# Kernel optimization log

Hardware: AMD Instinct MI355X
Metric: run time of the kernel (lower is better)

The kernel has to match this reference:

```python
import jax, jax.numpy as jnp
import numpy as np

TEMPERATURE = 0.5
EPS = 1e-20


def setup_inputs() -> dict:
    key = jax.random.key(0)
    ks = jax.random.split(key, 7)
    N, T, S = 16, 64, 1024
    SRC, TGT, D = 512, 512, 64
    return {
        "input": jax.random.normal(ks[0], (N, T, TGT), jnp.float32),
        "memory_bank": jax.random.normal(ks[1], (N, S, SRC), jnp.float32),
        "W_q": jax.random.normal(ks[2], (TGT, D), jnp.float32) / np.sqrt(TGT),
        "W_ctx": jax.random.normal(ks[3], (SRC, D), jnp.float32) / np.sqrt(SRC),
        "v": jax.random.normal(ks[4], (D,), jnp.float32) / np.sqrt(D),
        "W_out": jax.random.normal(ks[5], (SRC + TGT, TGT), jnp.float32) / np.sqrt(SRC + TGT),
        "b_out": jax.random.normal(ks[6], (TGT,), jnp.float32) * 0.01,
    }


def reference(input, memory_bank, W_q, W_ctx, v, W_out, b_out):
    # MLP attention score: v^T tanh(W_q q + W_ctx h)
    wq = jnp.einsum("ntd,de->nte", input, W_q)            # [N,T,D]
    uh = jnp.einsum("nsd,de->nse", memory_bank, W_ctx)    # [N,S,D]
    wquh = jnp.tanh(wq[:, :, None, :] + uh[:, None, :, :])  # [N,T,S,D]
    scores = jnp.einsum("ntsd,d->nts", wquh, v)           # [N,T,S]

    log_alpha = jax.nn.log_softmax(scores, axis=-1)
    alpha = jnp.exp(log_alpha)                            # c_align_vectors

    # deterministic context + output
    context_c = jnp.einsum("nts,nsd->ntd", alpha, memory_bank)
    h_c = jnp.tanh(jnp.concatenate([input, context_c], axis=-1) @ W_out + b_out)

    # gumbel-softmax sample (K = n_samples = 1, forced by view_as in original)
    u = jax.random.uniform(jax.random.key(42), log_alpha.shape, jnp.float32)
    g = -jnp.log(-jnp.log(u + EPS) + EPS)                 # gumbel noise
    y_align = jax.nn.softmax((log_alpha + g) / TEMPERATURE, axis=-1)  # [N,T,S]

    context_y = jnp.einsum("nts,nsd->ntd", y_align, memory_bank)
    h_y = jnp.tanh(jnp.concatenate([input, context_y], axis=-1) @ W_out + b_out)

    return jnp.stack([h_c, h_y], axis=0)  # [2,N,T,tgt_dim]
```

## Files before the change

kernel.cpp:

```cpp
#include <hip/hip_runtime.h>
#include <hip/hip_bf16.h>
#include <stdint.h>

#define DEV __device__ __forceinline__

typedef __attribute__((ext_vector_type(8))) short short8;
typedef __attribute__((ext_vector_type(4))) float f32x4;

#define TWO_LOG2E 2.8853900817779268f

DEV unsigned short f2bf(float f) {
  uint32_t u = __float_as_uint(f);
  u += 0x7FFFu + ((u >> 16) & 1u);
  return (unsigned short)(u >> 16);
}

DEV uint2 pk4(float4 f) {
  union { __hip_bfloat162 h; unsigned u; } a, b;
  a.h = __float22bfloat162_rn(make_float2(f.x, f.y));
  b.h = __float22bfloat162_rn(make_float2(f.z, f.w));
  return make_uint2(a.u, b.u);
}

DEV short8 mk8(uint2 lo, uint2 hi) {
  union { short8 s; uint4 u; } t;
  t.u = make_uint4(lo.x, lo.y, hi.x, hi.y);
  return t.s;
}

DEV uint32_t rotl32(uint32_t x, int r) { return (x << r) | (x >> (32 - r)); }

DEV void threefry_0_42(uint32_t x0, uint32_t x1, uint32_t& o0, uint32_t& o1) {
  const uint32_t ks0 = 0u, ks1 = 42u, ks2 = 0x1BD11BDAu ^ 42u;
  x0 += ks0; x1 += ks1;
#define TFR(r) { x0 += x1; x1 = rotl32(x1, (r)); x1 ^= x0; }
  TFR(13) TFR(15) TFR(26) TFR(6)  x0 += ks1; x1 += ks2 + 1u;
  TFR(17) TFR(29) TFR(16) TFR(24) x0 += ks2; x1 += ks0 + 2u;
  TFR(13) TFR(15) TFR(26) TFR(6)  x0 += ks0; x1 += ks1 + 3u;
  TFR(17) TFR(29) TFR(16) TFR(24) x0 += ks1; x1 += ks2 + 4u;
  TFR(13) TFR(15) TFR(26) TFR(6)  x0 += ks2; x1 += ks0 + 5u;
#undef TFR
  o0 = x0; o1 = x1;
}

DEV float wredmax(float v) {
#pragma unroll
  for (int off = 32; off > 0; off >>= 1) v = fmaxf(v, __shfl_xor(v, off));
  return v;
}
DEV float wredsum(float v) {
#pragma unroll
  for (int off = 32; off > 0; off >>= 1) v += __shfl_xor(v, off);
  return v;
}

DEV void ph_transpose(int b, int tid, char* smem,
                      const float* Wctx, const float* Wq, const float* Wout,
                      unsigned short* WctxT, unsigned short* WqT, unsigned short* WoutT) {
  float (*tile)[65] = (float(*)[65])smem;
  const float* src; unsigned short* dst; int R, C, br, bc;
  if (b < 8)       { src = Wctx; dst = WctxT; R = 512;  C = 64;  br = b * 64;       bc = 0; }
  else if (b < 16) { src = Wq;   dst = WqT;   R = 512;  C = 64;  br = (b - 8) * 64; bc = 0; }
  else { int i = b - 16; src = Wout; dst = WoutT; R = 1024; C = 512; br = (i & 15) * 64; bc = (i >> 4) * 64; }
  const int lr = tid >> 4, lc4 = (tid & 15) * 4;
#pragma unroll
  for (int i = 0; i < 4; ++i) {
    float4 vv = *(const float4*)(src + (long)(br + lr + i * 16) * C + bc + lc4);
    tile[lr + i * 16][lc4 + 0] = vv.x;
    tile[lr + i * 16][lc4 + 1] = vv.y;
    tile[lr + i * 16][lc4 + 2] = vv.z;
    tile[lr + i * 16][lc4 + 3] = vv.w;
  }
  __syncthreads();
#pragma unroll
  for (int i = 0; i < 4; ++i) {
    int crow = lr + i * 16;
    ushort4 o;
    o.x = f2bf(tile[lc4 + 0][crow]);
    o.y = f2bf(tile[lc4 + 1][crow]);
    o.z = f2bf(tile[lc4 + 2][crow]);
    o.w = f2bf(tile[lc4 + 3][crow]);
    *(ushort4*)(dst + (long)(bc + crow) * R + br + lc4) = o;
  }
}

DEV void ph_mbtile(int i, int tid, char* smem, const float* mb, unsigned short* mbT) {
  float (*tile)[65] = (float(*)[65])smem;
  const int n = i >> 7, rem = i & 127;
  const int sr0 = (rem >> 3) * 64;
  const int c0 = (rem & 7) * 64;
  const int lr = tid >> 4, lc4 = (tid & 15) * 4;
#pragma unroll
  for (int k = 0; k < 4; ++k) {
    float4 vv = *(const float4*)(mb + ((long)n * 1024 + sr0 + lr + k * 16) * 512 + c0 + lc4);
    tile[lr + k * 16][lc4 + 0] = vv.x;
    tile[lr + k * 16][lc4 + 1] = vv.y;
    tile[lr + k * 16][lc4 + 2] = vv.z;
    tile[lr + k * 16][lc4 + 3] = vv.w;
  }
  __syncthreads();
#pragma unroll
  for (int k = 0; k < 4; ++k) {
    int crow = lr + k * 16;
    ushort4 o;
    o.x = f2bf(tile[lc4 + 0][crow]);
    o.y = f2bf(tile[lc4 + 1][crow]);
    o.z = f2bf(tile[lc4 + 2][crow]);
    o.w = f2bf(tile[lc4 + 3][crow]);
    *(ushort4*)(mbT + (long)n * 524288 + (long)(c0 + crow) * 1024 + sr0 + lc4) = o;
  }
}

DEV void ph_uhwq(int t, int tid, char* smem,
                 const float* mb, const float* input,
                 const unsigned short* WctxT, const unsigned short* WqT,
                 float* uhT, float* wqo) {
  unsigned short (*As)[32] = (unsigned short(*)[32])smem;
  unsigned short (*Bs)[32] = (unsigned short(*)[32])(smem + 4096);
  const float* A; const unsigned short* BT; int mbase;
  if (t < 256) { A = mb;    BT = WctxT; mbase = t * 64; }
  else         { A = input; BT = WqT;   mbase = (t - 256) * 64; }
  const int srow = tid >> 2, kc = tid & 3;
  const int scol = ((kc ^ (srow & 3)) * 8);
  const int wave = tid >> 6, lane = tid & 63;
  const int wm = (wave >> 1) * 32, wn = (wave & 1) * 32;
  const int q = lane >> 4, r = lane & 15;
  const int c0 = ((q ^ (r & 3)) * 8);
  const float* ap = A + (long)(mbase + srow) * 512 + kc * 8;
  const unsigned short* bp = BT + (long)srow * 512 + kc * 8;
  f32x4 acc[2][2];
#pragma unroll
  for (int i = 0; i < 2; ++i)
#pragma unroll
    for (int j = 0; j < 2; ++j) acc[i][j] = (f32x4){0.f, 0.f, 0.f, 0.f};
  float4 fa0 = *(const float4*)(ap);
  float4 fa1 = *(const float4*)(ap + 4);
  uint4 fb = *(const uint4*)(bp);
  for (int k0 = 0; k0 < 512; k0 += 32) {
    uint2 p0 = pk4(fa0), p1 = pk4(fa1);
    *(uint4*)&As[srow][scol] = make_uint4(p0.x, p0.y, p1.x, p1.y);
    *(uint4*)&Bs[srow][scol] = fb;
    __syncthreads();
    if (k0 + 32 < 512) {
      fa0 = *(const float4*)(ap + k0 + 32);
      fa1 = *(const float4*)(ap + k0 + 36);
      fb = *(const uint4*)(bp + k0 + 32);
    }
    short8 a0 = *(const short8*)&As[wm + r][c0];
    short8 a1 = *(const short8*)&As[wm + 16 + r][c0];
    short8 b0 = *(const short8*)&Bs[wn + r][c0];
    short8 b1 = *(const short8*)&Bs[wn + 16 + r][c0];
    acc[0][0] = __builtin_amdgcn_mfma_f32_16x16x32_bf16(a0, b0, acc[0][0], 0, 0, 0);
    acc[0][1] = __builtin_amdgcn_mfma_f32_16x16x32_bf16(a0, b1, acc[0][1], 0, 0, 0);
    acc[1][0] = __builtin_amdgcn_mfma_f32_16x16x32_bf16(a1, b0, acc[1][0], 0, 0, 0);
    acc[1][1] = __builtin_amdgcn_mfma_f32_16x16x32_bf16(a1, b1, acc[1][1], 0, 0, 0);
    __syncthreads();
  }
#pragma unroll
  for (int i2 = 0; i2 < 2; ++i2)
#pragma unroll
    for (int j2 = 0; j2 < 2; ++j2) {
      int gcol = wn + j2 * 16 + r;
      int m = mbase + wm + i2 * 16 + q * 4;
      if (t < 256) {
        int n = m >> 10, s0 = m & 1023;
        float4 o;
        o.x = acc[i2][j2][0] * TWO_LOG2E;
        o.y = acc[i2][j2][1] * TWO_LOG2E;
        o.z = acc[i2][j2][2] * TWO_LOG2E;
        o.w = acc[i2][j2][3] * TWO_LOG2E;
        *(float4*)(uhT + (long)n * 65536 + (long)gcol * 1024 + s0) = o;
      } else {
#pragma unroll
        for (int reg = 0; reg < 4; ++reg)
          wqo[(long)(m + reg) * 64 + gcol] = acc[i2][j2][reg] * TWO_LOG2E;
      }
    }
}

DEV void ph_pre(int tt, int tid, char* smem,
                const float* input, const unsigned short* WoutT,
                const float* bout, float* P) {
  unsigned short (*As)[32] = (unsigned short(*)[32])smem;
  unsigned short (*Bs)[32] = (unsigned short(*)[32])(smem + 4096);
  const int mbase = (tt >> 4) * 64, nbase = (tt & 15) * 32;
  const int srow = tid >> 2, kc = tid & 3;
  const int scol = ((kc ^ (srow & 3)) * 8);
  const int wave = tid >> 6, lane = tid & 63;
  const int wm = (wave >> 1) * 32, wn = (wave & 1) * 16;
  const int q = lane >> 4, r = lane & 15;
  const int c0 = ((q ^ (r & 3)) * 8);
  const float* ap = input + (long)(mbase + srow) * 512 + kc * 8;
  const int brow = (tid & 127) >> 2;
  const unsigned short* bp = WoutT + (long)(nbase + brow) * 1024 + kc * 8;
  f32x4 acc[2];
  acc[0] = (f32x4){0.f, 0.f, 0.f, 0.f};
  acc[1] = (f32x4){0.f, 0.f, 0.f, 0.f};
  float4 fa0 = *(const float4*)(ap);
  float4 fa1 = *(const float4*)(ap + 4);
  uint4 fb;
  if (tid < 128) fb = *(const uint4*)(bp);
  for (int k0 = 0; k0 < 512; k0 += 32) {
    uint2 p0 = pk4(fa0), p1 = pk4(fa1);
    *(uint4*)&As[srow][scol] = make_uint4(p0.x, p0.y, p1.x, p1.y);
    if (tid < 128) *(uint4*)&Bs[brow][(kc ^ (brow & 3)) * 8] = fb;
    __syncthreads();
    int kn = k0 + 32;
    if (kn < 512) {
      fa0 = *(const float4*)(ap + kn);
      fa1 = *(const float4*)(ap + kn + 4);
      if (tid < 128) fb = *(const uint4*)(bp + kn);
    }
    short8 a0 = *(const short8*)&As[wm + r][c0];
    short8 a1 = *(const short8*)&As[wm + 16 + r][c0];
    short8 b0 = *(const short8*)&Bs[wn + r][c0];
    acc[0] = __builtin_amdgcn_mfma_f32_16x16x32_bf16(a0, b0, acc[0], 0, 0, 0);
    acc[1] = __builtin_amdgcn_mfma_f32_16x16x32_bf16(a1, b0, acc[1], 0, 0, 0);
    __syncthreads();
  }
#pragma unroll
  for (int i2 = 0; i2 < 2; ++i2) {
    int gcol = nbase + wn + r;
    float bb = bout[gcol];
#pragma unroll
    for (int reg = 0; reg < 4; ++reg) {
      int grow = mbase + wm + i2 * 16 + q * 4 + reg;
      P[(long)grow * 512 + gcol] = acc[i2][reg] + bb;
    }
  }
}

DEV void softmax_gumbel_write(float* lsc, int nt, int tid, float* red,
                              unsigned short* alpha_bf, unsigned short* yal_bf) {
  const int wv = tid >> 6, ln = tid & 63;
  float m = fmaxf(fmaxf(lsc[0], lsc[1]), fmaxf(lsc[2], lsc[3]));
  m = wredmax(m);
  if (ln == 0) red[wv] = m;
  __syncthreads();
  m = fmaxf(fmaxf(red[0], red[1]), fmaxf(red[2], red[3]));
  __syncthreads();
  float ss = 0.f;
#pragma unroll
  for (int i = 0; i < 4; ++i) ss += __expf(lsc[i] - m);
  ss = wredsum(ss);
  if (ln == 0) red[wv] = ss;
  __syncthreads();
  ss = red[0] + red[1] + red[2] + red[3];
  const float logl = __logf(ss);
  __syncthreads();

  const uint32_t jbase = (uint32_t)nt * 1024u + (uint32_t)tid * 4u;
  float ys[4];
  float4 av;
#pragma unroll
  for (int i = 0; i < 4; ++i) {
    float la = lsc[i] - m - logl;
    ((float*)&av)[i] = __expf(la);
    uint32_t o0, o1;
    threefry_0_42(0u, jbase + i, o0, o1);
    uint32_t bits = o0 ^ o1;
    float u = __uint_as_float((bits >> 9) | 0x3f800000u) - 1.0f;
    float g = -__logf(-__logf(u + 1e-20f) + 1e-20f);
    ys[i] = (la + g) * 2.0f;
  }
  {
    uint2 pa = pk4(av);
    *(uint2*)(alpha_bf + (long)nt * 1024 + tid * 4) = pa;
  }
  float m2 = fmaxf(fmaxf(ys[0], ys[1]), fmaxf(ys[2], ys[3]));
  m2 = wredmax(m2);
  if (ln == 0) red[wv] = m2;
  __syncthreads();
  m2 = fmaxf(fmaxf(red[0], red[1]), fmaxf(red[2], red[3]));
  __syncthreads();
  float s2 = 0.f;
  float4 ye;
#pragma unroll
  for (int i = 0; i < 4; ++i) { ((float*)&ye)[i] = __expf(ys[i] - m2); s2 += ((float*)&ye)[i]; }
  s2 = wredsum(s2);
  if (ln == 0) red[wv] = s2;
  __syncthreads();
  s2 = red[0] + red[1] + red[2] + red[3];
  const float rinv = __fdividef(1.f, s2);
  ye.x *= rinv; ye.y *= rinv; ye.z *= rinv; ye.w *= rinv;
  {
    uint2 py = pk4(ye);
    *(uint2*)(yal_bf + (long)nt * 1024 + tid * 4) = py;
  }
  __syncthreads();
}

DEV void ph_scores_pair(int nt0, int tid, char* smem,
                        const float* uhT, const float* wqo, const float* vvec,
                        unsigned short* alpha_bf, unsigned short* yal_bf) {
  float* wvs0 = (float*)smem;
  float* wvs1 = wvs0 + 64;
  float* vvs  = wvs1 + 64;
  float* red  = vvs + 64;
  const int nt1 = nt0 + 512;
  const int n0 = nt0 >> 6, n1 = nt1 >> 6;
  if (tid < 64) {
    wvs0[tid] = wqo[nt0 * 64 + tid];
    wvs1[tid] = wqo[nt1 * 64 + tid];
    vvs[tid]  = vvec[tid];
  }
  __syncthreads();
  float sumv = 0.f;
#pragma unroll
  for (int d = 0; d < 64; d += 4) {
    float4 vv = *(const float4*)&vvs[d];
    sumv += vv.x + vv.y + vv.z + vv.w;
  }
  const float* un0 = uhT + (long)n0 * 65536 + tid * 4;
  const float* un1 = uhT + (long)n1 * 65536 + tid * 4;
  float4 r0 = make_float4(0.f, 0.f, 0.f, 0.f);
  float4 r1 = make_float4(0.f, 0.f, 0.f, 0.f);
  for (int db = 0; db < 64; db += 4) {
    float4 ua[4], ub[4];
#pragma unroll
    for (int j = 0; j < 4; ++j) {
      ua[j] = *(const float4*)(un0 + (long)(db + j) * 1024);
      ub[j] = *(const float4*)(un1 + (long)(db + j) * 1024);
    }
#pragma unroll
    for (int j = 0; j < 4; ++j) {
      float w0 = wvs0[db + j], w1 = wvs1[db + j], vvj = vvs[db + j];
      r0.x = fmaf(vvj, __builtin_amdgcn_rcpf(1.f + __builtin_amdgcn_exp2f(ua[j].x + w0)), r0.x);
      r0.y = fmaf(vvj, __builtin_amdgcn_rcpf(1.f + __builtin_amdgcn_exp2f(ua[j].y + w0)), r0.y);
      r0.z = fmaf(vvj, __builtin_amdgcn_rcpf(1.f + __builtin_amdgcn_exp2f(ua[j].z + w0)), r0.z);
      r0.w = fmaf(vvj, __builtin_amdgcn_rcpf(1.f + __builtin_amdgcn_exp2f(ua[j].w + w0)), r0.w);
      r1.x = fmaf(vvj, __builtin_amdgcn_rcpf(1.f + __builtin_amdgcn_exp2f(ub[j].x + w1)), r1.x);
      r1.y = fmaf(vvj, __builtin_amdgcn_rcpf(1.f + __builtin_amdgcn_exp2f(ub[j].y + w1)), r1.y);
      r1.z = fmaf(vvj, __builtin_amdgcn_rcpf(1.f + __builtin_amdgcn_exp2f(ub[j].z + w1)), r1.z);
      r1.w = fmaf(vvj, __builtin_amdgcn_rcpf(1.f + __builtin_amdgcn_exp2f(ub[j].w + w1)), r1.w);
    }
  }
  float lsc0[4], lsc1[4];
  lsc0[0] = fmaf(-2.f, r0.x, sumv); lsc0[1] = fmaf(-2.f, r0.y, sumv);
  lsc0[2] = fmaf(-2.f, r0.z, sumv); lsc0[3] = fmaf(-2.f, r0.w, sumv);
  lsc1[0] = fmaf(-2.f, r1.x, sumv); lsc1[1] = fmaf(-2.f, r1.y, sumv);
  lsc1[2] = fmaf(-2.f, r1.z, sumv); lsc1[3] = fmaf(-2.f, r1.w, sumv);
  softmax_gumbel_write(lsc0, nt0, tid, red, alpha_bf, yal_bf);
  softmax_gumbel_write(lsc1, nt1, tid, red, alpha_bf, yal_bf);
}

DEV void ph_ctx_fast(int n, int dbase, int vt, int tid, char* smem,
                     const unsigned short* alpha_bf, const unsigned short* yal_bf,
                     const unsigned short* mbT, unsigned short* ctxb) {
  unsigned short (*As)[32] = (unsigned short(*)[32])smem;
  const int srow = tid >> 2, kc = tid & 3;
  const int scol = ((kc ^ (srow & 3)) * 8);
  const int wave = tid >> 6, lane = tid & 63;
  const int wm = (wave >> 1) * 32, wn = (wave & 1) * 16;
  const int q = lane >> 4, r = lane & 15;
  const int c0 = ((q ^ (r & 3)) * 8);
  const unsigned short* Ab = (vt ? yal_bf : alpha_bf) + (long)n * 65536 + (long)srow * 1024 + kc * 8;
  const unsigned short* Bb = mbT + (long)n * 524288 + (long)(dbase + wn + r) * 1024 + q * 8;
  f32x4 acc[2];
  acc[0] = (f32x4){0.f, 0.f, 0.f, 0.f};
  acc[1] = (f32x4){0.f, 0.f, 0.f, 0.f};
  uint4 fa  = *(const uint4*)(Ab);
  uint4 fb0 = *(const uint4*)(Bb);
  uint4 fb1 = *(const uint4*)(Bb + 32);
  for (int k0 = 0; k0 < 1024; k0 += 32) {
    *(uint4*)&As[srow][scol] = fa;
    __syncthreads();
    union { uint4 u; short8 s; } bu; bu.u = fb0;
    if (k0 + 32 < 1024) fa = *(const uint4*)(Ab + k0 + 32);
    fb0 = fb1;
    if (k0 + 64 < 1024) fb1 = *(const uint4*)(Bb + k0 + 64);
    short8 a0 = *(const short8*)&As[wm + r][c0];
    short8 a1 = *(const short8*)&As[wm + 16 + r][c0];
    acc[0] = __builtin_amdgcn_mfma_f32_16x16x32_bf16(a0, bu.s, acc[0], 0, 0, 0);
    acc[1] = __builtin_amdgcn_mfma_f32_16x16x32_bf16(a1, bu.s, acc[1], 0, 0, 0);
    __syncthreads();
  }
#pragma unroll
  for (int i2 = 0; i2 < 2; ++i2) {
    int gcol = dbase + wn + r;
#pragma unroll
    for (int reg = 0; reg < 4; ++reg) {
      long grow = (long)vt * 1024 + n * 64 + wm + i2 * 16 + q * 4 + reg;
      ctxb[grow * 512 + gcol] = f2bf(acc[i2][reg]);
    }
  }
}

DEV void ph_ctx_legacy(int n, int dbase, int vt, int tid, char* smem,
                       const unsigned short* alpha_bf, const unsigned short* yal_bf,
                       const float* mb, unsigned short* ctxb) {
  unsigned short (*As)[32] = (unsigned short(*)[32])smem;
  const int srow = tid >> 2, kc = tid & 3;
  const int scol = ((kc ^ (srow & 3)) * 8);
  const int wave = tid >> 6, lane = tid & 63;
  const int wm = (wave >> 1) * 32, wn = (wave & 1) * 16;
  const int q = lane >> 4, r = lane & 15;
  const int c0 = ((q ^ (r & 3)) * 8);
  const unsigned short* Ab = (vt ? yal_bf : alpha_bf) + (long)n * 65536 + (long)srow * 1024 + kc * 8;
  const float* bcol = mb + (long)n * 524288 + dbase + wn + r;
  f32x4 acc[2];
  acc[0] = (f32x4){0.f, 0.f, 0.f, 0.f};
  acc[1] = (f32x4){0.f, 0.f, 0.f, 0.f};
  uint4 fa = *(const uint4*)(Ab);
  float bv[8];
#pragma unroll
  for (int j = 0; j < 8; ++j) bv[j] = bcol[(long)(q * 8 + j) * 512];
  for (int k0 = 0; k0 < 1024; k0 += 32) {
    *(uint4*)&As[srow][scol] = fa;
    __syncthreads();
    float4 blo = make_float4(bv[0], bv[1], bv[2], bv[3]);
    float4 bhi = make_float4(bv[4], bv[5], bv[6], bv[7]);
    short8 b0 = mk8(pk4(blo), pk4(bhi));
    if (k0 + 32 < 1024) {
      fa = *(const uint4*)(Ab + k0 + 32);
#pragma unroll
      for (int j = 0; j < 8; ++j) bv[j] = bcol[(long)(k0 + 32 + q * 8 + j) * 512];
    }
    short8 a0 = *(const short8*)&As[wm + r][c0];
    short8 a1 = *(const short8*)&As[wm + 16 + r][c0];
    acc[0] = __builtin_amdgcn_mfma_f32_16x16x32_bf16(a0, b0, acc[0], 0, 0, 0);
    acc[1] = __builtin_amdgcn_mfma_f32_16x16x32_bf16(a1, b0, acc[1], 0, 0, 0);
    __syncthreads();
  }
#pragma unroll
  for (int i2 = 0; i2 < 2; ++i2) {
    int gcol = dbase + wn + r;
#pragma unroll
    for (int reg = 0; reg < 4; ++reg) {
      long grow = (long)vt * 1024 + n * 64 + wm + i2 * 16 + q * 4 + reg;
      ctxb[grow * 512 + gcol] = f2bf(acc[i2][reg]);
    }
  }
}

DEV void ph_out(int mbase, int nbase, int tid, char* smem,
                const unsigned short* ctxb, const unsigned short* WoutT,
                const float* P, float* out) {
  unsigned short (*As)[32] = (unsigned short(*)[32])smem;
  unsigned short (*Bs)[32] = (unsigned short(*)[32])(smem + 4096);
  const int srow = tid >> 2, kc = tid & 3;
  const int scol = ((kc ^ (srow & 3)) * 8);
  const int wave = tid >> 6, lane = tid & 63;
  const int wm = (wave >> 1) * 32, wn = (wave & 1) * 16;
  const int q = lane >> 4, r = lane & 15;
  const int c0 = ((q ^ (r & 3)) * 8);
  const unsigned short* ap = ctxb + (long)(mbase + srow) * 512 + kc * 8;
  const int brow = (tid & 127) >> 2;
  const unsigned short* bp = WoutT + (long)(nbase + brow) * 1024 + 512 + kc * 8;
  f32x4 acc[2];
#pragma unroll
  for (int i2 = 0; i2 < 2; ++i2) {
    int pcol = nbase + wn + r;
#pragma unroll
    for (int reg = 0; reg < 4; ++reg) {
      int prow = (mbase + wm + i2 * 16 + q * 4 + reg) & 1023;
      acc[i2][reg] = P[(long)prow * 512 + pcol];
    }
  }
  uint4 fa = *(const uint4*)(ap);
  uint4 fb;
  if (tid < 128) fb = *(const uint4*)(bp);
  for (int k0 = 0; k0 < 512; k0 += 32) {
    *(uint4*)&As[srow][scol] = fa;
    if (tid < 128) *(uint4*)&Bs[brow][(kc ^ (brow & 3)) * 8] = fb;
    __syncthreads();
    int kn = k0 + 32;
    if (kn < 512) {
      fa = *(const uint4*)(ap + kn);
      if (tid < 128) fb = *(const uint4*)(bp + kn);
    }
    short8 a0 = *(const short8*)&As[wm + r][c0];
    short8 a1 = *(const short8*)&As[wm + 16 + r][c0];
    short8 b0 = *(const short8*)&Bs[wn + r][c0];
    acc[0] = __builtin_amdgcn_mfma_f32_16x16x32_bf16(a0, b0, acc[0], 0, 0, 0);
    acc[1] = __builtin_amdgcn_mfma_f32_16x16x32_bf16(a1, b0, acc[1], 0, 0, 0);
    __syncthreads();
  }
#pragma unroll
  for (int i2 = 0; i2 < 2; ++i2) {
    int gcol = nbase + wn + r;
#pragma unroll
    for (int reg = 0; reg < 4; ++reg) {
      int grow = mbase + wm + i2 * 16 + q * 4 + reg;
      float z = acc[i2][reg];
      float rc = __builtin_amdgcn_rcpf(1.f + __builtin_amdgcn_exp2f(z * TWO_LOG2E));
      out[(long)grow * 512 + gcol] = fmaf(-2.f, rc, 1.f);
    }
  }
}

__global__ __launch_bounds__(256) void k_prep(const float* __restrict__ Wctx,
                                              const float* __restrict__ Wq,
                                              const float* __restrict__ Wout,
                                              const float* __restrict__ mb,
                                              unsigned short* __restrict__ WctxT,
                                              unsigned short* __restrict__ WqT,
                                              unsigned short* __restrict__ WoutT,
                                              unsigned short* __restrict__ mbT) {
  __shared__ __align__(16) char smem[16640];
  const int b = blockIdx.x;
  if (b < 144) ph_transpose(b, threadIdx.x, smem, Wctx, Wq, Wout, WctxT, WqT, WoutT);
  else         ph_mbtile(b - 144, threadIdx.x, smem, mb, mbT);
}

__global__ __launch_bounds__(256) void k_uhwq_pre(const float* __restrict__ mb,
                                                  const float* __restrict__ input,
                                                  const unsigned short* __restrict__ WctxT,
                                                  const unsigned short* __restrict__ WqT,
                                                  const unsigned short* __restrict__ WoutT,
                                                  const float* __restrict__ bout,
                                                  float* __restrict__ uhT,
                                                  float* __restrict__ wqo,
                                                  float* __restrict__ P) {
  __shared__ __align__(16) char smem[8192];
  const int b = blockIdx.x;
  if (b < 272) ph_uhwq(b, threadIdx.x, smem, mb, input, WctxT, WqT, uhT, wqo);
  else         ph_pre(b - 272, threadIdx.x, smem, input, WoutT, bout, P);
}

__global__ __launch_bounds__(256) void k_scores(const float* __restrict__ uhT,
                                                const float* __restrict__ wqo,
                                                const float* __restrict__ vvec,
                                                unsigned short* __restrict__ alpha_bf,
                                                unsigned short* __restrict__ yal_bf) {
  __shared__ __align__(16) char smem[1024];
  ph_scores_pair(blockIdx.x, threadIdx.x, smem, uhT, wqo, vvec, alpha_bf, yal_bf);
}

__global__ __launch_bounds__(256) void k_ctx_fast(const unsigned short* __restrict__ alpha_bf,
                                                  const unsigned short* __restrict__ yal_bf,
                                                  const unsigned short* __restrict__ mbT,
                                                  unsigned short* __restrict__ ctxb) {
  __shared__ __align__(16) char smem[4096];
  const int x = blockIdx.x;
  ph_ctx_fast(x & 15, ((x >> 4) & 15) * 32, x >> 8, threadIdx.x, smem, alpha_bf, yal_bf, mbT, ctxb);
}

__global__ __launch_bounds__(256) void k_ctx_legacy(const unsigned short* __restrict__ alpha_bf,
                                                    const unsigned short* __restrict__ yal_bf,
                                                    const float* __restrict__ mb,
                                                    unsigned short* __restrict__ ctxb) {
  __shared__ __align__(16) char smem[4096];
  const int x = blockIdx.x;
  ph_ctx_legacy(x & 15, ((x >> 4) & 15) * 32, x >> 8, threadIdx.x, smem, alpha_bf, yal_bf, mb, ctxb);
}

__global__ __launch_bounds__(256) void k_out(const unsigned short* __restrict__ ctxb,
                                             const unsigned short* __restrict__ WoutT,
                                             const float* __restrict__ P,
                                             float* __restrict__ out) {
  __shared__ __align__(16) char smem[8192];
  ph_out((blockIdx.x >> 4) * 64, (blockIdx.x & 15) * 32, threadIdx.x, smem, ctxb, WoutT, P, out);
}

extern "C" void kernel_launch(void* const* d_in, const int* in_sizes, int n_in,
                              void* d_out, int out_size, void* d_ws, size_t ws_size,
                              hipStream_t stream) {
  const float* input = (const float*)d_in[0];
  const float* mb    = (const float*)d_in[1];
  const float* W_q   = (const float*)d_in[2];
  const float* W_ctx = (const float*)d_in[3];
  const float* v     = (const float*)d_in[4];
  const float* W_out = (const float*)d_in[5];
  const float* b_out = (const float*)d_in[6];
  float* out = (float*)d_out;
  float* ws = (float*)d_ws;

  float* uhT = ws;
  float* wqo = ws + 1048576;
  unsigned short* alpha_bf = (unsigned short*)(ws + 1114112);
  unsigned short* yal_bf   = (unsigned short*)(ws + 1638400);
  unsigned short* WctxT = (unsigned short*)(ws + 2162688);
  unsigned short* WqT   = (unsigned short*)(ws + 2179072);
  unsigned short* WoutT = (unsigned short*)(ws + 2195456);
  unsigned short* ctxb  = (unsigned short*)(ws + 2457600);
  float* P = ws + 2981888;
  unsigned short* mbT = (unsigned short*)(ws + 3506176);

  const bool big = ws_size >= (size_t)7700480 * 4;

  k_prep<<<big ? 2192 : 144, 256, 0, stream>>>(W_ctx, W_q, W_out, mb, WctxT, WqT, WoutT, mbT);
  k_uhwq_pre<<<528, 256, 0, stream>>>(mb, input, WctxT, WqT, WoutT, b_out, uhT, wqo, P);
  k_scores<<<512, 256, 0, stream>>>(uhT, wqo, v, alpha_bf, yal_bf);
  if (big) k_ctx_fast<<<512, 256, 0, stream>>>(alpha_bf, yal_bf, mbT, ctxb);
  else     k_ctx_legacy<<<512, 256, 0, stream>>>(alpha_bf, yal_bf, mb, ctxb);
  k_out<<<512, 256, 0, stream>>>(ctxb, WoutT, P, out);
}
```

Baseline: 147.6 us.

## Pre-convert inputs to bf16 and stage GEMM tiles via async global-to-LDS double buffering

```diff
diff --git a/kernel.cpp b/kernel.cpp
--- a/kernel.cpp
+++ b/kernel.cpp
@@ -8,6 +8,7 @@
 typedef __attribute__((ext_vector_type(4))) float f32x4;
 
 #define TWO_LOG2E 2.8853900817779268f
+#define MFMA16(a, b, c) __builtin_amdgcn_mfma_f32_16x16x32_bf16((a), (b), (c), 0, 0, 0)
 
 DEV unsigned short f2bf(float f) {
   uint32_t u = __float_as_uint(f);
@@ -20,12 +21,6 @@
   a.h = __float22bfloat162_rn(make_float2(f.x, f.y));
   b.h = __float22bfloat162_rn(make_float2(f.z, f.w));
   return make_uint2(a.u, b.u);
-}
-
-DEV short8 mk8(uint2 lo, uint2 hi) {
-  union { short8 s; uint4 u; } t;
-  t.u = make_uint4(lo.x, lo.y, hi.x, hi.y);
-  return t.s;
 }
 
 DEV uint32_t rotl32(uint32_t x, int r) { return (x << r) | (x >> (32 - r)); }
@@ -54,6 +49,34 @@
   return v;
 }
 
+DEV void gld16(const unsigned short* g, unsigned short* l) {
+  __builtin_amdgcn_global_load_lds(
+      (__attribute__((address_space(1))) void*)g,
+      (__attribute__((address_space(3))) void*)l, 16, 0, 0);
+}
+
+DEV void stage64(const unsigned short* src, long lda, int k0,
+                 unsigned short* buf, int tid) {
+  const int srow = tid >> 2;
+  const int sc = (((tid & 3) ^ (srow & 3)) * 8);
+  const int wave = tid >> 6;
+  const unsigned short* g = src + (long)srow * lda + k0 + sc;
+  gld16(g,      buf + wave * 512);
+  gld16(g + 32, buf + 2048 + wave * 512);
+}
+
+DEV void stage32(const unsigned short* src, long lda, int k0,
+                 unsigned short* buf, int tid) {
+  const int wave = tid >> 6, lane = tid & 63;
+  const int h = wave >> 1;
+  const int row = ((wave & 1) << 4) + (lane >> 2);
+  const int sc = (((lane & 3) ^ (row & 3)) * 8);
+  gld16(src + (long)row * lda + k0 + h * 32 + sc,
+        buf + h * 1024 + (wave & 1) * 512);
+}
+
+#define RD8(buf, row, col) (*(const short8*)&(buf)[(row) * 32 + (col)])
+
 DEV void ph_transpose(int b, int tid, char* smem,
                       const float* Wctx, const float* Wq, const float* Wout,
                       unsigned short* WctxT, unsigned short* WqT, unsigned short* WoutT) {
@@ -84,7 +107,8 @@
   }
 }
 
-DEV void ph_mbtile(int i, int tid, char* smem, const float* mb, unsigned short* mbT) {
+DEV void ph_mbtile(int i, int tid, char* smem, const float* mb,
+                   unsigned short* mbT, unsigned short* mb_bf) {
   float (*tile)[65] = (float(*)[65])smem;
   const int n = i >> 7, rem = i & 127;
   const int sr0 = (rem >> 3) * 64;
@@ -92,11 +116,15 @@
   const int lr = tid >> 4, lc4 = (tid & 15) * 4;
 #pragma unroll
   for (int k = 0; k < 4; ++k) {
-    float4 vv = *(const float4*)(mb + ((long)n * 1024 + sr0 + lr + k * 16) * 512 + c0 + lc4);
+    const long srow = (long)n * 1024 + sr0 + lr + k * 16;
+    float4 vv = *(const float4*)(mb + srow * 512 + c0 + lc4);
     tile[lr + k * 16][lc4 + 0] = vv.x;
     tile[lr + k * 16][lc4 + 1] = vv.y;
     tile[lr + k * 16][lc4 + 2] = vv.z;
     tile[lr + k * 16][lc4 + 3] = vv.w;
+    ushort4 o;
+    o.x = f2bf(vv.x); o.y = f2bf(vv.y); o.z = f2bf(vv.z); o.w = f2bf(vv.w);
+    *(ushort4*)(mb_bf + srow * 512 + c0 + lc4) = o;
   }
   __syncthreads();
 #pragma unroll
@@ -111,121 +139,142 @@
   }
 }
 
-DEV void ph_uhwq(int t, int tid, char* smem,
-                 const float* mb, const float* input,
-                 const unsigned short* WctxT, const unsigned short* WqT,
-                 float* uhT, float* wqo) {
-  unsigned short (*As)[32] = (unsigned short(*)[32])smem;
-  unsigned short (*Bs)[32] = (unsigned short(*)[32])(smem + 4096);
-  const float* A; const unsigned short* BT; int mbase;
-  if (t < 256) { A = mb;    BT = WctxT; mbase = t * 64; }
-  else         { A = input; BT = WqT;   mbase = (t - 256) * 64; }
-  const int srow = tid >> 2, kc = tid & 3;
-  const int scol = ((kc ^ (srow & 3)) * 8);
+DEV void ph_inpconv(int i, int tid, const float* input, unsigned short* input_bf) {
+  const long base = (long)i * 8192 + (long)tid * 32;
+#pragma unroll
+  for (int j = 0; j < 32; j += 4) {
+    float4 vv = *(const float4*)(input + base + j);
+    uint2 p = pk4(vv);
+    *(uint2*)(input_bf + base + j) = p;
+  }
+}
+
+__global__ __launch_bounds__(256) void k_prep(const float* __restrict__ Wctx,
+                                              const float* __restrict__ Wq,
+                                              const float* __restrict__ Wout,
+                                              const float* __restrict__ mb,
+                                              const float* __restrict__ input,
+                                              unsigned short* __restrict__ WctxT,
+                                              unsigned short* __restrict__ WqT,
+                                              unsigned short* __restrict__ WoutT,
+                                              unsigned short* __restrict__ mbT,
+                                              unsigned short* __restrict__ mb_bf,
+                                              unsigned short* __restrict__ input_bf) {
+  __shared__ __align__(16) char smem[16640];
+  const int b = blockIdx.x;
+  if (b < 144)       ph_transpose(b, threadIdx.x, smem, Wctx, Wq, Wout, WctxT, WqT, WoutT);
+  else if (b < 2192) ph_mbtile(b - 144, threadIdx.x, smem, mb, mbT, mb_bf);
+  else               ph_inpconv(b - 2192, threadIdx.x, input, input_bf);
+}
+
+__global__ __launch_bounds__(256) void k_gemms(const unsigned short* __restrict__ mb_bf,
+                                               const unsigned short* __restrict__ input_bf,
+                                               const unsigned short* __restrict__ WctxT,
+                                               const unsigned short* __restrict__ WqT,
+                                               const unsigned short* __restrict__ WoutT,
+                                               const float* __restrict__ bout,
+                                               float* __restrict__ uhT,
+                                               float* __restrict__ wqo,
+                                               float* __restrict__ P) {
+  __shared__ __align__(16) unsigned short Ab[8192];
+  __shared__ __align__(16) unsigned short Bb[8192];
+  const int tid = threadIdx.x;
+  const int t = blockIdx.x;
   const int wave = tid >> 6, lane = tid & 63;
-  const int wm = (wave >> 1) * 32, wn = (wave & 1) * 32;
   const int q = lane >> 4, r = lane & 15;
   const int c0 = ((q ^ (r & 3)) * 8);
-  const float* ap = A + (long)(mbase + srow) * 512 + kc * 8;
-  const unsigned short* bp = BT + (long)srow * 512 + kc * 8;
-  f32x4 acc[2][2];
-#pragma unroll
-  for (int i = 0; i < 2; ++i)
-#pragma unroll
-    for (int j = 0; j < 2; ++j) acc[i][j] = (f32x4){0.f, 0.f, 0.f, 0.f};
-  float4 fa0 = *(const float4*)(ap);
-  float4 fa1 = *(const float4*)(ap + 4);
-  uint4 fb = *(const uint4*)(bp);
-  for (int k0 = 0; k0 < 512; k0 += 32) {
-    uint2 p0 = pk4(fa0), p1 = pk4(fa1);
-    *(uint4*)&As[srow][scol] = make_uint4(p0.x, p0.y, p1.x, p1.y);
-    *(uint4*)&Bs[srow][scol] = fb;
-    __syncthreads();
-    if (k0 + 32 < 512) {
-      fa0 = *(const float4*)(ap + k0 + 32);
-      fa1 = *(const float4*)(ap + k0 + 36);
-      fb = *(const uint4*)(bp + k0 + 32);
-    }
-    short8 a0 = *(const short8*)&As[wm + r][c0];
-    short8 a1 = *(const short8*)&As[wm + 16 + r][c0];
-    short8 b0 = *(const short8*)&Bs[wn + r][c0];
-    short8 b1 = *(const short8*)&Bs[wn + 16 + r][c0];
-    acc[0][0] = __builtin_amdgcn_mfma_f32_16x16x32_bf16(a0, b0, acc[0][0], 0, 0, 0);
-    acc[0][1] = __builtin_amdgcn_mfma_f32_16x16x32_bf16(a0, b1, acc[0][1], 0, 0, 0);
-    acc[1][0] = __builtin_amdgcn_mfma_f32_16x16x32_bf16(a1, b0, acc[1][0], 0, 0, 0);
-    acc[1][1] = __builtin_amdgcn_mfma_f32_16x16x32_bf16(a1, b1, acc[1][1], 0, 0, 0);
-    __syncthreads();
-  }
-#pragma unroll
-  for (int i2 = 0; i2 < 2; ++i2)
-#pragma unroll
-    for (int j2 = 0; j2 < 2; ++j2) {
-      int gcol = wn + j2 * 16 + r;
-      int m = mbase + wm + i2 * 16 + q * 4;
-      if (t < 256) {
-        int n = m >> 10, s0 = m & 1023;
-        float4 o;
-        o.x = acc[i2][j2][0] * TWO_LOG2E;
-        o.y = acc[i2][j2][1] * TWO_LOG2E;
-        o.z = acc[i2][j2][2] * TWO_LOG2E;
-        o.w = acc[i2][j2][3] * TWO_LOG2E;
-        *(float4*)(uhT + (long)n * 65536 + (long)gcol * 1024 + s0) = o;
-      } else {
-#pragma unroll
-        for (int reg = 0; reg < 4; ++reg)
-          wqo[(long)(m + reg) * 64 + gcol] = acc[i2][j2][reg] * TWO_LOG2E;
+
+  if (t < 272) {
+    const unsigned short* Asrc; const unsigned short* Bsrc; int mbase;
+    if (t < 256) { Asrc = mb_bf + (long)t * 32768;          Bsrc = WctxT; mbase = t * 64; }
+    else         { Asrc = input_bf + (long)(t - 256) * 32768; Bsrc = WqT; mbase = (t - 256) * 64; }
+    const int wm = (wave >> 1) * 32, wn = (wave & 1) * 32;
+    f32x4 acc[2][2];
+#pragma unroll
+    for (int i = 0; i < 2; ++i)
+#pragma unroll
+      for (int j = 0; j < 2; ++j) acc[i][j] = (f32x4){0.f, 0.f, 0.f, 0.f};
+    stage64(Asrc, 512, 0, Ab, tid);
+    stage64(Bsrc, 512, 0, Bb, tid);
+    for (int c = 0; c < 8; ++c) {
+      const int db = (c & 1) * 4096;
+      __syncthreads();
+      if (c < 7) {
+        stage64(Asrc, 512, (c + 1) * 64, Ab + (db ^ 4096), tid);
+        stage64(Bsrc, 512, (c + 1) * 64, Bb + (db ^ 4096), tid);
       }
-    }
-}
-
-DEV void ph_pre(int tt, int tid, char* smem,
-                const float* input, const unsigned short* WoutT,
-                const float* bout, float* P) {
-  unsigned short (*As)[32] = (unsigned short(*)[32])smem;
-  unsigned short (*Bs)[32] = (unsigned short(*)[32])(smem + 4096);
-  const int mbase = (tt >> 4) * 64, nbase = (tt & 15) * 32;
-  const int srow = tid >> 2, kc = tid & 3;
-  const int scol = ((kc ^ (srow & 3)) * 8);
-  const int wave = tid >> 6, lane = tid & 63;
-  const int wm = (wave >> 1) * 32, wn = (wave & 1) * 16;
-  const int q = lane >> 4, r = lane & 15;
-  const int c0 = ((q ^ (r & 3)) * 8);
-  const float* ap = input + (long)(mbase + srow) * 512 + kc * 8;
-  const int brow = (tid & 127) >> 2;
-  const unsigned short* bp = WoutT + (long)(nbase + brow) * 1024 + kc * 8;
-  f32x4 acc[2];
-  acc[0] = (f32x4){0.f, 0.f, 0.f, 0.f};
-  acc[1] = (f32x4){0.f, 0.f, 0.f, 0.f};
-  float4 fa0 = *(const float4*)(ap);
-  float4 fa1 = *(const float4*)(ap + 4);
-  uint4 fb;
-  if (tid < 128) fb = *(const uint4*)(bp);
-  for (int k0 = 0; k0 < 512; k0 += 32) {
-    uint2 p0 = pk4(fa0), p1 = pk4(fa1);
-    *(uint4*)&As[srow][scol] = make_uint4(p0.x, p0.y, p1.x, p1.y);
-    if (tid < 128) *(uint4*)&Bs[brow][(kc ^ (brow & 3)) * 8] = fb;
-    __syncthreads();
-    int kn = k0 + 32;
-    if (kn < 512) {
-      fa0 = *(const float4*)(ap + kn);
-      fa1 = *(const float4*)(ap + kn + 4);
-      if (tid < 128) fb = *(const uint4*)(bp + kn);
-    }
-    short8 a0 = *(const short8*)&As[wm + r][c0];
-    short8 a1 = *(const short8*)&As[wm + 16 + r][c0];
-    short8 b0 = *(const short8*)&Bs[wn + r][c0];
-    acc[0] = __builtin_amdgcn_mfma_f32_16x16x32_bf16(a0, b0, acc[0], 0, 0, 0);
-    acc[1] = __builtin_amdgcn_mfma_f32_16x16x32_bf16(a1, b0, acc[1], 0, 0, 0);
-    __syncthreads();
-  }
-#pragma unroll
-  for (int i2 = 0; i2 < 2; ++i2) {
-    int gcol = nbase + wn + r;
-    float bb = bout[gcol];
-#pragma unroll
-    for (int reg = 0; reg < 4; ++reg) {
-      int grow = mbase + wm + i2 * 16 + q * 4 + reg;
-      P[(long)grow * 512 + gcol] = acc[i2][reg] + bb;
+#pragma unroll
+      for (int h = 0; h < 2; ++h) {
+        const unsigned short* A = Ab + db + h * 2048;
+        const unsigned short* B = Bb + db + h * 2048;
+        short8 a0 = RD8(A, wm + r, c0);
+        short8 a1 = RD8(A, wm + 16 + r, c0);
+        short8 b0 = RD8(B, wn + r, c0);
+        short8 b1 = RD8(B, wn + 16 + r, c0);
+        acc[0][0] = MFMA16(a0, b0, acc[0][0]);
+        acc[0][1] = MFMA16(a0, b1, acc[0][1]);
+        acc[1][0] = MFMA16(a1, b0, acc[1][0]);
+        acc[1][1] = MFMA16(a1, b1, acc[1][1]);
+      }
+    }
+#pragma unroll
+    for (int i2 = 0; i2 < 2; ++i2)
+#pragma unroll
+      for (int j2 = 0; j2 < 2; ++j2) {
+        int gcol = wn + j2 * 16 + r;
+        int m = mbase + wm + i2 * 16 + q * 4;
+        if (t < 256) {
+          int n = m >> 10, s0 = m & 1023;
+          float4 o;
+          o.x = acc[i2][j2][0] * TWO_LOG2E;
+          o.y = acc[i2][j2][1] * TWO_LOG2E;
+          o.z = acc[i2][j2][2] * TWO_LOG2E;
+          o.w = acc[i2][j2][3] * TWO_LOG2E;
+          *(float4*)(uhT + (long)n * 65536 + (long)gcol * 1024 + s0) = o;
+        } else {
+#pragma unroll
+          for (int reg = 0; reg < 4; ++reg)
+            wqo[(long)(m + reg) * 64 + gcol] = acc[i2][j2][reg] * TWO_LOG2E;
+        }
+      }
+  } else {
+    const int tt = t - 272;
+    const int mbase = (tt >> 4) * 64, nbase = (tt & 15) * 32;
+    const int wm = (wave >> 1) * 32, wn = (wave & 1) * 16;
+    const unsigned short* Asrc = input_bf + (long)mbase * 512;
+    const unsigned short* Bsrc = WoutT + (long)nbase * 1024;
+    f32x4 acc[2];
+    acc[0] = (f32x4){0.f, 0.f, 0.f, 0.f};
+    acc[1] = (f32x4){0.f, 0.f, 0.f, 0.f};
+    stage64(Asrc, 512, 0, Ab, tid);
+    stage32(Bsrc, 1024, 0, Bb, tid);
+    for (int c = 0; c < 8; ++c) {
+      const int dbA = (c & 1) * 4096, dbB = (c & 1) * 2048;
+      __syncthreads();
+      if (c < 7) {
+        stage64(Asrc, 512, (c + 1) * 64, Ab + (dbA ^ 4096), tid);
+        stage32(Bsrc, 1024, (c + 1) * 64, Bb + (dbB ^ 2048), tid);
+      }
+#pragma unroll
+      for (int h = 0; h < 2; ++h) {
+        const unsigned short* A = Ab + dbA + h * 2048;
+        const unsigned short* B = Bb + dbB + h * 1024;
+        short8 a0 = RD8(A, wm + r, c0);
+        short8 a1 = RD8(A, wm + 16 + r, c0);
+        short8 b0 = RD8(B, wn + r, c0);
+        acc[0] = MFMA16(a0, b0, acc[0]);
+        acc[1] = MFMA16(a1, b0, acc[1]);
+      }
+    }
+#pragma unroll
+    for (int i2 = 0; i2 < 2; ++i2) {
+      int gcol = nbase + wn + r;
+      float bb = bout[gcol];
+#pragma unroll
+      for (int reg = 0; reg < 4; ++reg) {
+        int grow = mbase + wm + i2 * 16 + q * 4 + reg;
+        P[(long)grow * 512 + gcol] = acc[i2][reg] + bb;
+      }
     }
   }
 }
@@ -290,13 +339,19 @@
   __syncthreads();
 }
 
-DEV void ph_scores_pair(int nt0, int tid, char* smem,
-                        const float* uhT, const float* wqo, const float* vvec,
-                        unsigned short* alpha_bf, unsigned short* yal_bf) {
-  float* wvs0 = (float*)smem;
-  float* wvs1 = wvs0 + 64;
-  float* vvs  = wvs1 + 64;
-  float* red  = vvs + 64;
+__global__ __launch_bounds__(256) void k_scores(const float* __restrict__ uhT,
+                                                const float* __restrict__ wqo,
+                                                const float* __restrict__ vvec,
+                                                unsigned short* __restrict__ alpha_bf,
+                                                unsigned short* __restrict__ yal_bf) {
+  __shared__ __align__(16) float smf[196];
+  float* wvs0 = smf;
+  float* wvs1 = smf + 64;
+  float* vvs  = smf + 128;
+  float* red  = smf + 192;
+  const int tid = threadIdx.x;
+  const int bid = blockIdx.x;
+  const int nt0 = ((bid & 7) << 6) | (bid >> 3);
   const int nt1 = nt0 + 512;
   const int n0 = nt0 >> 6, n1 = nt1 >> 6;
   if (tid < 64) {
@@ -344,36 +399,44 @@
   softmax_gumbel_write(lsc1, nt1, tid, red, alpha_bf, yal_bf);
 }
 
-DEV void ph_ctx_fast(int n, int dbase, int vt, int tid, char* smem,
-                     const unsigned short* alpha_bf, const unsigned short* yal_bf,
-                     const unsigned short* mbT, unsigned short* ctxb) {
-  unsigned short (*As)[32] = (unsigned short(*)[32])smem;
-  const int srow = tid >> 2, kc = tid & 3;
-  const int scol = ((kc ^ (srow & 3)) * 8);
+__global__ __launch_bounds__(256) void k_ctx(const unsigned short* __restrict__ alpha_bf,
+                                             const unsigned short* __restrict__ yal_bf,
+                                             const unsigned short* __restrict__ mbT,
+                                             unsigned short* __restrict__ ctxb) {
+  __shared__ __align__(16) unsigned short Ab[8192];
+  const int tid = threadIdx.x;
+  const int x = blockIdx.x;
+  const int n = x & 15, dbase = ((x >> 4) & 15) * 32, vt = x >> 8;
   const int wave = tid >> 6, lane = tid & 63;
   const int wm = (wave >> 1) * 32, wn = (wave & 1) * 16;
   const int q = lane >> 4, r = lane & 15;
   const int c0 = ((q ^ (r & 3)) * 8);
-  const unsigned short* Ab = (vt ? yal_bf : alpha_bf) + (long)n * 65536 + (long)srow * 1024 + kc * 8;
-  const unsigned short* Bb = mbT + (long)n * 524288 + (long)(dbase + wn + r) * 1024 + q * 8;
+  const unsigned short* Asrc = (vt ? yal_bf : alpha_bf) + (long)n * 65536;
+  const unsigned short* Bp = mbT + (long)n * 524288 + (long)(dbase + wn + r) * 1024 + q * 8;
   f32x4 acc[2];
   acc[0] = (f32x4){0.f, 0.f, 0.f, 0.f};
   acc[1] = (f32x4){0.f, 0.f, 0.f, 0.f};
-  uint4 fa  = *(const uint4*)(Ab);
-  uint4 fb0 = *(const uint4*)(Bb);
-  uint4 fb1 = *(const uint4*)(Bb + 32);
-  for (int k0 = 0; k0 < 1024; k0 += 32) {
-    *(uint4*)&As[srow][scol] = fa;
+  stage64(Asrc, 1024, 0, Ab, tid);
+  uint4 nb0 = *(const uint4*)(Bp);
+  uint4 nb1 = *(const uint4*)(Bp + 32);
+  for (int c = 0; c < 16; ++c) {
+    const int db = (c & 1) * 4096;
     __syncthreads();
-    union { uint4 u; short8 s; } bu; bu.u = fb0;
-    if (k0 + 32 < 1024) fa = *(const uint4*)(Ab + k0 + 32);
-    fb0 = fb1;
-    if (k0 + 64 < 1024) fb1 = *(const uint4*)(Bb + k0 + 64);
-    short8 a0 = *(const short8*)&As[wm + r][c0];
-    short8 a1 = *(const short8*)&As[wm + 16 + r][c0];
-    acc[0] = __builtin_amdgcn_mfma_f32_16x16x32_bf16(a0, bu.s, acc[0], 0, 0, 0);
-    acc[1] = __builtin_amdgcn_mfma_f32_16x16x32_bf16(a1, bu.s, acc[1], 0, 0, 0);
-    __syncthreads();
+    if (c < 15) stage64(Asrc, 1024, (c + 1) * 64, Ab + (db ^ 4096), tid);
+    union { uint4 u; short8 s; } B0, B1;
+    B0.u = nb0; B1.u = nb1;
+    if (c < 15) {
+      nb0 = *(const uint4*)(Bp + (c + 1) * 64);
+      nb1 = *(const uint4*)(Bp + (c + 1) * 64 + 32);
+    }
+    short8 a0 = RD8(Ab + db, wm + r, c0);
+    short8 a1 = RD8(Ab + db, wm + 16 + r, c0);
+    acc[0] = MFMA16(a0, B0.s, acc[0]);
+    acc[1] = MFMA16(a1, B0.s, acc[1]);
+    a0 = RD8(Ab + db + 2048, wm + r, c0);
+    a1 = RD8(Ab + db + 2048, wm + 16 + r, c0);
+    acc[0] = MFMA16(a0, B1.s, acc[0]);
+    acc[1] = MFMA16(a1, B1.s, acc[1]);
   }
 #pragma unroll
   for (int i2 = 0; i2 < 2; ++i2) {
@@ -386,67 +449,20 @@
   }
 }
 
-DEV void ph_ctx_legacy(int n, int dbase, int vt, int tid, char* smem,
-                       const unsigned short* alpha_bf, const unsigned short* yal_bf,
-                       const float* mb, unsigned short* ctxb) {
-  unsigned short (*As)[32] = (unsigned short(*)[32])smem;
-  const int srow = tid >> 2, kc = tid & 3;
-  const int scol = ((kc ^ (srow & 3)) * 8);
+__global__ __launch_bounds__(256) void k_out(const unsigned short* __restrict__ ctxb,
+                                             const unsigned short* __restrict__ WoutT,
+                                             const float* __restrict__ P,
+                                             float* __restrict__ out) {
+  __shared__ __align__(16) unsigned short Ab[8192];
+  __shared__ __align__(16) unsigned short Bb[4096];
+  const int tid = threadIdx.x;
+  const int mbase = (blockIdx.x >> 4) * 64, nbase = (blockIdx.x & 15) * 32;
   const int wave = tid >> 6, lane = tid & 63;
   const int wm = (wave >> 1) * 32, wn = (wave & 1) * 16;
   const int q = lane >> 4, r = lane & 15;
   const int c0 = ((q ^ (r & 3)) * 8);
-  const unsigned short* Ab = (vt ? yal_bf : alpha_bf) + (long)n * 65536 + (long)srow * 1024 + kc * 8;
-  const float* bcol = mb + (long)n * 524288 + dbase + wn + r;
-  f32x4 acc[2];
-  acc[0] = (f32x4){0.f, 0.f, 0.f, 0.f};
-  acc[1] = (f32x4){0.f, 0.f, 0.f, 0.f};
-  uint4 fa = *(const uint4*)(Ab);
-  float bv[8];
-#pragma unroll
-  for (int j = 0; j < 8; ++j) bv[j] = bcol[(long)(q * 8 + j) * 512];
-  for (int k0 = 0; k0 < 1024; k0 += 32) {
-    *(uint4*)&As[srow][scol] = fa;
-    __syncthreads();
-    float4 blo = make_float4(bv[0], bv[1], bv[2], bv[3]);
-    float4 bhi = make_float4(bv[4], bv[5], bv[6], bv[7]);
-    short8 b0 = mk8(pk4(blo), pk4(bhi));
-    if (k0 + 32 < 1024) {
-      fa = *(const uint4*)(Ab + k0 + 32);
-#pragma unroll
-      for (int j = 0; j < 8; ++j) bv[j] = bcol[(long)(k0 + 32 + q * 8 + j) * 512];
-    }
-    short8 a0 = *(const short8*)&As[wm + r][c0];
-    short8 a1 = *(const short8*)&As[wm + 16 + r][c0];
-    acc[0] = __builtin_amdgcn_mfma_f32_16x16x32_bf16(a0, b0, acc[0], 0, 0, 0);
-    acc[1] = __builtin_amdgcn_mfma_f32_16x16x32_bf16(a1, b0, acc[1], 0, 0, 0);
-    __syncthreads();
-  }
-#pragma unroll
-  for (int i2 = 0; i2 < 2; ++i2) {
-    int gcol = dbase + wn + r;
-#pragma unroll
-    for (int reg = 0; reg < 4; ++reg) {
-      long grow = (long)vt * 1024 + n * 64 + wm + i2 * 16 + q * 4 + reg;
-      ctxb[grow * 512 + gcol] = f2bf(acc[i2][reg]);
-    }
-  }
-}
-
-DEV void ph_out(int mbase, int nbase, int tid, char* smem,
-                const unsigned short* ctxb, const unsigned short* WoutT,
-                const float* P, float* out) {
-  unsigned short (*As)[32] = (unsigned short(*)[32])smem;
-  unsigned short (*Bs)[32] = (unsigned short(*)[32])(smem + 4096);
-  const int srow = tid >> 2, kc = tid & 3;
-  const int scol = ((kc ^ (srow & 3)) * 8);
-  const int wave = tid >> 6, lane = tid & 63;
-  const int wm = (wave >> 1) * 32, wn = (wave & 1) * 16;
-  const int q = lane >> 4, r = lane & 15;
-  const int c0 = ((q ^ (r & 3)) * 8);
-  const unsigned short* ap = ctxb + (long)(mbase + srow) * 512 + kc * 8;
-  const int brow = (tid & 127) >> 2;
-  const unsigned short* bp = WoutT + (long)(nbase + brow) * 1024 + 512 + kc * 8;
+  const unsigned short* Asrc = ctxb + (long)mbase * 512;
+  const unsigned short* Bsrc = WoutT + (long)nbase * 1024 + 512;
   f32x4 acc[2];
 #pragma unroll
   for (int i2 = 0; i2 < 2; ++i2) {
@@ -457,24 +473,25 @@
       acc[i2][reg] = P[(long)prow * 512 + pcol];
     }
   }
-  uint4 fa = *(const uint4*)(ap);
-  uint4 fb;
-  if (tid < 128) fb = *(const uint4*)(bp);
-  for (int k0 = 0; k0 < 512; k0 += 32) {
-    *(uint4*)&As[srow][scol] = fa;
-    if (tid < 128) *(uint4*)&Bs[brow][(kc ^ (brow & 3)) * 8] = fb;
+  stage64(Asrc, 512, 0, Ab, tid);
+  stage32(Bsrc, 1024, 0, Bb, tid);
+  for (int c = 0; c < 8; ++c) {
+    const int dbA = (c & 1) * 4096, dbB = (c & 1) * 2048;
     __syncthreads();
-    int kn = k0 + 32;
-    if (kn < 512) {
-      fa = *(const uint4*)(ap + kn);
-      if (tid < 128) fb = *(const uint4*)(bp + kn);
-    }
-    short8 a0 = *(const short8*)&As[wm + r][c0];
-    short8 a1 = *(const short8*)&As[wm + 16 + r][c0];
-    short8 b0 = *(const short8*)&Bs[wn + r][c0];
-    acc[0] = __builtin_amdgcn_mfma_f32_16x16x32_bf16(a0, b0, acc[0], 0, 0, 0);
-    acc[1] = __builtin_amdgcn_mfma_f32_16x16x32_bf16(a1, b0, acc[1], 0, 0, 0);
-    __syncthreads();
+    if (c < 7) {
+      stage64(Asrc, 512, (c + 1) * 64, Ab + (dbA ^ 4096), tid);
+      stage32(Bsrc, 1024, (c + 1) * 64, Bb + (dbB ^ 2048), tid);
+    }
+#pragma unroll
+    for (int h = 0; h < 2; ++h) {
+      const unsigned short* A = Ab + dbA + h * 2048;
+      const unsigned short* B = Bb + dbB + h * 1024;
+      short8 a0 = RD8(A, wm + r, c0);
+      short8 a1 = RD8(A, wm + 16 + r, c0);
+      short8 b0 = RD8(B, wn + r, c0);
+      acc[0] = MFMA16(a0, b0, acc[0]);
+      acc[1] = MFMA16(a1, b0, acc[1]);
+    }
   }
 #pragma unroll
   for (int i2 = 0; i2 < 2; ++i2) {
@@ -487,70 +504,6 @@
       out[(long)grow * 512 + gcol] = fmaf(-2.f, rc, 1.f);
     }
   }
-}
-
-__global__ __launch_bounds__(256) void k_prep(const float* __restrict__ Wctx,
-                                              const float* __restrict__ Wq,
-                                              const float* __restrict__ Wout,
-                                              const float* __restrict__ mb,
-                                              unsigned short* __restrict__ WctxT,
-                                              unsigned short* __restrict__ WqT,
-                                              unsigned short* __restrict__ WoutT,
-                                              unsigned short* __restrict__ mbT) {
-  __shared__ __align__(16) char smem[16640];
-  const int b = blockIdx.x;
-  if (b < 144) ph_transpose(b, threadIdx.x, smem, Wctx, Wq, Wout, WctxT, WqT, WoutT);
-  else         ph_mbtile(b - 144, threadIdx.x, smem, mb, mbT);
-}
-
-__global__ __launch_bounds__(256) void k_uhwq_pre(const float* __restrict__ mb,
-                                                  const float* __restrict__ input,
-                                                  const unsigned short* __restrict__ WctxT,
-                                                  const unsigned short* __restrict__ WqT,
-                                                  const unsigned short* __restrict__ WoutT,
-                                                  const float* __restrict__ bout,
-                                                  float* __restrict__ uhT,
-                                                  float* __restrict__ wqo,
-                                                  float* __restrict__ P) {
-  __shared__ __align__(16) char smem[8192];
-  const int b = blockIdx.x;
-  if (b < 272) ph_uhwq(b, threadIdx.x, smem, mb, input, WctxT, WqT, uhT, wqo);
-  else         ph_pre(b - 272, threadIdx.x, smem, input, WoutT, bout, P);
-}
-
-__global__ __launch_bounds__(256) void k_scores(const float* __restrict__ uhT,
-                                                const float* __restrict__ wqo,
-                                                const float* __restrict__ vvec,
-                                                unsigned short* __restrict__ alpha_bf,
-                                                unsigned short* __restrict__ yal_bf) {
-  __shared__ __align__(16) char smem[1024];
-  ph_scores_pair(blockIdx.x, threadIdx.x, smem, uhT, wqo, vvec, alpha_bf, yal_bf);
-}
-
-__global__ __launch_bounds__(256) void k_ctx_fast(const unsigned short* __restrict__ alpha_bf,
-                                                  const unsigned short* __restrict__ yal_bf,
-                                                  const unsigned short* __restrict__ mbT,
-                                                  unsigned short* __restrict__ ctxb) {
-  __shared__ __align__(16) char smem[4096];
-  const int x = blockIdx.x;
-  ph_ctx_fast(x & 15, ((x >> 4) & 15) * 32, x >> 8, threadIdx.x, smem, alpha_bf, yal_bf, mbT, ctxb);
-}
-
-__global__ __launch_bounds__(256) void k_ctx_legacy(const unsigned short* __restrict__ alpha_bf,
-                                                    const unsigned short* __restrict__ yal_bf,
-                                                    const float* __restrict__ mb,
-                                                    unsigned short* __restrict__ ctxb) {
-  __shared__ __align__(16) char smem[4096];
-  const int x = blockIdx.x;
-  ph_ctx_legacy(x & 15, ((x >> 4) & 15) * 32, x >> 8, threadIdx.x, smem, alpha_bf, yal_bf, mb, ctxb);
-}
-
-__global__ __launch_bounds__(256) void k_out(const unsigned short* __restrict__ ctxb,
-                                             const unsigned short* __restrict__ WoutT,
-                                             const float* __restrict__ P,
-                                             float* __restrict__ out) {
-  __shared__ __align__(16) char smem[8192];
-  ph_out((blockIdx.x >> 4) * 64, (blockIdx.x & 15) * 32, threadIdx.x, smem, ctxb, WoutT, P, out);
 }
 
 extern "C" void kernel_launch(void* const* d_in, const int* in_sizes, int n_in,
@@ -575,14 +528,14 @@
   unsigned short* WoutT = (unsigned short*)(ws + 2195456);
   unsigned short* ctxb  = (unsigned short*)(ws + 2457600);
   float* P = ws + 2981888;
-  unsigned short* mbT = (unsigned short*)(ws + 3506176);
-
-  const bool big = ws_size >= (size_t)7700480 * 4;
-
-  k_prep<<<big ? 2192 : 144, 256, 0, stream>>>(W_ctx, W_q, W_out, mb, WctxT, WqT, WoutT, mbT);
-  k_uhwq_pre<<<528, 256, 0, stream>>>(mb, input, WctxT, WqT, WoutT, b_out, uhT, wqo, P);
+  unsigned short* mbT      = (unsigned short*)(ws + 3506176);
+  unsigned short* mb_bf    = (unsigned short*)(ws + 7700480);
+  unsigned short* input_bf = (unsigned short*)(ws + 11894784);
+
+  k_prep<<<2256, 256, 0, stream>>>(W_ctx, W_q, W_out, mb, input,
+                                   WctxT, WqT, WoutT, mbT, mb_bf, input_bf);
+  k_gemms<<<528, 256, 0, stream>>>(mb_bf, input_bf, WctxT, WqT, WoutT, b_out, uhT, wqo, P);
   k_scores<<<512, 256, 0, stream>>>(uhT, wqo, v, alpha_bf, yal_bf);
-  if (big) k_ctx_fast<<<512, 256, 0, stream>>>(alpha_bf, yal_bf, mbT, ctxb);
-  else     k_ctx_legacy<<<512, 256, 0, stream>>>(alpha_bf, yal_bf, mb, ctxb);
+  k_ctx<<<512, 256, 0, stream>>>(alpha_bf, yal_bf, mbT, ctxb);
   k_out<<<512, 256, 0, stream>>>(ctxb, WoutT, P, out);
 }
```

After: 150.3 us. No clear change (+1.8%).
